# Performance work log

Measured on AMD Instinct MI355X. Metric: run time of the kernel, lower is better.

## Reference

```python
import jax, jax.numpy as jnp
import numpy as np

N_NODES = 100000


def _sage_conv(x, src, dst, W_l, b_l, W_r, n_nodes):
    # mean-aggregate neighbor features: messages flow src -> dst
    msg = x[src]                                              # [E, d]
    agg_sum = jax.ops.segment_sum(msg, dst, num_segments=n_nodes)   # [N, d]
    cnt = jax.ops.segment_sum(jnp.ones((src.shape[0],), x.dtype), dst,
                              num_segments=n_nodes)           # [N]
    agg = agg_sum / jnp.maximum(cnt, 1.0)[:, None]            # mean, 0 for isolated nodes
    return agg @ W_l + b_l + x @ W_r                          # lin_l(agg) + lin_r(x)


def setup_inputs() -> dict:
    key = jax.random.key(0)
    ks = jax.random.split(key, 8)
    in_c, hid_c, out_c = 64, 128, 64
    n_edges = 1000000
    x = jax.random.normal(ks[0], (N_NODES, in_c), dtype=jnp.float32)
    edge_index = jax.random.randint(ks[1], (2, n_edges), 0, N_NODES, dtype=jnp.int32)
    def glorot(k, shape):
        lim = float(np.sqrt(6.0 / (shape[0] + shape[1])))
        return jax.random.uniform(k, shape, jnp.float32, -lim, lim)
    return {
        "x": x,
        "edge_index": edge_index,
        "W_l1": glorot(ks[2], (in_c, hid_c)),
        "b_l1": jnp.zeros((hid_c,), jnp.float32),
        "W_r1": glorot(ks[3], (in_c, hid_c)),
        "W_l2": glorot(ks[4], (hid_c, out_c)),
        "b_l2": jnp.zeros((out_c,), jnp.float32),
        "W_r2": glorot(ks[5], (hid_c, out_c)),
    }


def reference(x, edge_index, W_l1, b_l1, W_r1, W_l2, b_l2, W_r2):
    src, dst = edge_index[0], edge_index[1]
    # eval mode: dropout(p=0.5) is identity
    h = _sage_conv(x, src, dst, W_l1, b_l1, W_r1, N_NODES)
    h = jax.nn.relu(h)
    out = _sage_conv(h, src, dst, W_l2, b_l2, W_r2, N_NODES)
    return out
```

## Files before the change

kernel.cpp:

```cpp
#include <hip/hip_runtime.h>


#define NPB 128
#define NBK 782
#define BCAP_E 1600
#define BCAP_S 2048

typedef __attribute__((ext_vector_type(8))) short bf16x8;
typedef __attribute__((ext_vector_type(4))) float f32x4;
typedef __attribute__((ext_vector_type(4))) int int4v;

__device__ __forceinline__ float bf2f(unsigned short u) {
  return __uint_as_float(((unsigned)u) << 16);
}
__device__ __forceinline__ unsigned short f2bf(float f) {
  unsigned x = __float_as_uint(f);
  x += 0x7fffu + ((x >> 16) & 1u);
  return (unsigned short)(x >> 16);
}

__global__ __launch_bounds__(256) void fused_misc(
    const float* __restrict__ x, unsigned short* __restrict__ xb, int total4,
    const float* __restrict__ Wl1, const float* __restrict__ Wr1,
    const float* __restrict__ Wl2, const float* __restrict__ Wr2,
    unsigned short* __restrict__ Wt1, unsigned short* __restrict__ Wcat,
    int* __restrict__ gcnt, unsigned short* __restrict__ agg1b,
    int n, int CB) {
  int b = blockIdx.x;
  if (b < CB) {
    int i = b * 256 + threadIdx.x;
    if (i < total4) {
      float4 v = ((const float4*)x)[i];
      ushort4 o;
      o.x = f2bf(v.x); o.y = f2bf(v.y); o.z = f2bf(v.z); o.w = f2bf(v.w);
      ((ushort4*)xb)[i] = o;
    }
  } else if (b < CB + 128) {
    int o = (b - CB) * 256 + threadIdx.x;
    if (o < 16384) {
      int m = o >> 13, rem = o & 8191;
      int col = rem >> 6, k = rem & 63;
      const float* W = m ? Wr1 : Wl1;
      Wt1[o] = f2bf(W[k * 128 + col]);
    } else {
      int o2 = o - 16384;
      int col = o2 >> 7, k = o2 & 127;
      float v = (col < 64) ? Wl2[k * 64 + col] : Wr2[k * 64 + col - 64];
      Wcat[o2] = f2bf(v);
    }
  } else {
    for (int i = threadIdx.x; i < NBK; i += 256) gcnt[i] = 0;
    if (threadIdx.x < 32) {
      ((unsigned*)(xb + (size_t)n * 64))[threadIdx.x] = 0;
      ((unsigned*)(agg1b + (size_t)n * 64))[threadIdx.x] = 0;
    }
  }
}

__global__ __launch_bounds__(256) void bucketize(
    const int* __restrict__ src, const int* __restrict__ dst,
    int* __restrict__ gcnt, int* __restrict__ ebuf, int e) {
  __shared__ int lcnt[NBK], lbase[NBK];
  for (int i = threadIdx.x; i < NBK; i += 256) lcnt[i] = 0;
  __syncthreads();
  int pk[16], bk[16];
  int nv = 0;
  int base = blockIdx.x * 4096 + threadIdx.x * 4;
#pragma unroll
  for (int c = 0; c < 4; ++c) {
    int i = base + c * 1024;
    if (i + 4 <= e) {
      int4v sv = *(const int4v*)(src + i);
      int4v dv = *(const int4v*)(dst + i);
#pragma unroll
      for (int j = 0; j < 4; ++j) {
        bk[nv] = dv[j] >> 7;
        pk[nv] = ((dv[j] & 127) << 17) | sv[j];
        ++nv;
      }
    } else if (i < e) {
      for (int i2 = i; i2 < e; ++i2) {
        int dj = dst[i2], sj = src[i2];
        bk[nv] = dj >> 7;
        pk[nv] = ((dj & 127) << 17) | sj;
        ++nv;
      }
    }
  }
  for (int k = 0; k < nv; ++k) atomicAdd(&lcnt[bk[k]], 1);
  __syncthreads();
  for (int i = threadIdx.x; i < NBK; i += 256) {
    lbase[i] = atomicAdd(&gcnt[i], lcnt[i]);
    lcnt[i] = 0;
  }
  __syncthreads();
  for (int k = 0; k < nv; ++k) {
    int off = lbase[bk[k]] + atomicAdd(&lcnt[bk[k]], 1);
    if (off < BCAP_E) ebuf[bk[k] * BCAP_E + off] = pk[k];
  }
}

__global__ __launch_bounds__(256) void sort_write(
    const int* __restrict__ gcnt, const int* __restrict__ ebuf,
    int* __restrict__ srcS, int* __restrict__ nstart, int* __restrict__ ncnt,
    int n) {
  __shared__ int cnt[NPB], cur[NPB], st[NPB + 1], sorted[BCAP_S];
  int tid = threadIdx.x, lane = tid & 63, wid = tid >> 6;
  int b = blockIdx.x;
  if (tid < NPB) { cnt[tid] = 0; cur[tid] = 0; }
  __syncthreads();
  int ecnt = min(gcnt[b], BCAP_E);
  const int* eb = ebuf + b * BCAP_E;
  for (int i = tid; i < ecnt; i += 256) atomicAdd(&cnt[eb[i] >> 17], 1);
  __syncthreads();
  if (wid == 0) {
    int i0 = (cnt[lane] + 3) & ~3, i1 = (cnt[64 + lane] + 3) & ~3;
#pragma unroll
    for (int off = 1; off < 64; off <<= 1) {
      int u = __shfl_up(i0, off);
      if (lane >= off) i0 += u;
    }
    int t0 = __shfl(i0, 63);
#pragma unroll
    for (int off = 1; off < 64; off <<= 1) {
      int u = __shfl_up(i1, off);
      if (lane >= off) i1 += u;
    }
    st[lane + 1] = i0;
    st[64 + lane + 1] = t0 + i1;
    if (lane == 0) st[0] = 0;
  }
  __syncthreads();
  for (int i = tid; i < ecnt; i += 256) {
    int pk = eb[i];
    int dl = pk >> 17;
    int pos = st[dl] + atomicAdd(&cur[dl], 1);
    if (pos < BCAP_S) sorted[pos] = pk & 0x1FFFF;
  }
  __syncthreads();
  if (tid < NPB) {
    int c = cnt[tid], p = (c + 3) & ~3;
    int base = st[tid];
    for (int k = c; k < p; ++k)
      if (base + k < BCAP_S) sorted[base + k] = n;
  }
  __syncthreads();
  int total = min(st[NPB], BCAP_S);
  for (int i = tid; i < total; i += 256) srcS[b * BCAP_S + i] = sorted[i];
  if (tid < NPB) {
    int node = b * NPB + tid;
    if (node < n) {
      nstart[node] = b * BCAP_S + st[tid];
      ncnt[node] = cnt[tid];
    }
  }
}

__device__ __forceinline__ void gather2(
    const unsigned short* __restrict__ feat, const int* __restrict__ srcS,
    int s, int dpad, int lane, float* acc) {
  int half32 = lane & 32;
  int hlane = lane & 31;
  int g = hlane >> 3;
  int ch8 = lane & 7;
#pragma unroll
  for (int j = 0; j < 8; ++j) acc[j] = 0.f;
  int nit = dpad >> 2;
  int nitw = max(nit, __shfl_xor(nit, 32));
  int idx = srcS[s + hlane];
  bf16x8 c[8];
#pragma unroll
  for (int u = 0; u < 8; ++u) {
    if (u < nitw) {
      int r = u * 4 + g;
      int sidx = __shfl(idx, half32 + r);
      if (u < nit) c[u] = *(const bf16x8*)(feat + (size_t)sidx * 64 + ch8 * 8);
    }
  }
#pragma unroll
  for (int u = 0; u < 8; ++u) {
    if (u < nitw && u < nit) {
#pragma unroll
      for (int j = 0; j < 8; ++j) acc[j] += bf2f((unsigned short)c[u][j]);
    }
  }
  for (int b0 = 32; b0 < dpad; b0 += 32) {
    int idx2 = srcS[s + b0 + hlane];
#pragma unroll
    for (int u = 0; u < 8; ++u) {
      int r = u * 4 + g;
      if (b0 + r < dpad) {
        int sidx = __shfl(idx2, half32 + r);
        bf16x8 v = *(const bf16x8*)(feat + (size_t)sidx * 64 + ch8 * 8);
#pragma unroll
        for (int j = 0; j < 8; ++j) acc[j] += bf2f((unsigned short)v[j]);
      }
    }
  }
#pragma unroll
  for (int m = 8; m < 32; m <<= 1) {
#pragma unroll
    for (int j = 0; j < 8; ++j) acc[j] += __shfl_xor(acc[j], m);
  }
}

__global__ __launch_bounds__(256) void agg_mean_fast(
    const unsigned short* __restrict__ feat, const int* __restrict__ nstart,
    const int* __restrict__ ncnt, const int* __restrict__ srcS,
    unsigned short* __restrict__ outp, int n) {
  int lane = threadIdx.x & 63, wid = threadIdx.x >> 6;
  int half = lane >> 5;
  int node = (blockIdx.x * 4 + wid) * 2 + half;
  bool live = node < n;
  int cn = live ? node : n - 1;
  int s = nstart[cn];
  int c = ncnt[cn];
  int dpad = (c + 3) & ~3;
  float acc[8];
  gather2(feat, srcS, s, dpad, lane, acc);
  float inv = 1.f / (float)max(c, 1);
  if ((lane & 31) < 8 && live) {
    bf16x8 o;
#pragma unroll
    for (int j = 0; j < 8; ++j) o[j] = (short)f2bf(acc[j] * inv);
    *(bf16x8*)(outp + (size_t)node * 64 + (lane & 7) * 8) = o;
  }
}

__global__ __launch_bounds__(256) void agg_add_fast(
    const unsigned short* __restrict__ feat, const int* __restrict__ nstart,
    const int* __restrict__ ncnt, const int* __restrict__ srcS,
    float* __restrict__ outp, int n) {
  int lane = threadIdx.x & 63, wid = threadIdx.x >> 6;
  int half = lane >> 5;
  int node = (blockIdx.x * 4 + wid) * 2 + half;
  bool live = node < n;
  int cn = live ? node : n - 1;
  int s = nstart[cn];
  int c = ncnt[cn];
  int dpad = (c + 3) & ~3;
  float acc[8];
  gather2(feat, srcS, s, dpad, lane, acc);
  float inv = 1.f / (float)max(c, 1);
  if ((lane & 31) < 8 && live) {
    float4* op = (float4*)(outp + (size_t)node * 64 + (lane & 7) * 8);
    float4 o0 = op[0], o1 = op[1];
    o0.x += acc[0] * inv; o0.y += acc[1] * inv;
    o0.z += acc[2] * inv; o0.w += acc[3] * inv;
    o1.x += acc[4] * inv; o1.y += acc[5] * inv;
    o1.z += acc[6] * inv; o1.w += acc[7] * inv;
    op[0] = o0; op[1] = o1;
  }
}

__global__ __launch_bounds__(256) void gemm1_mfma(
    const unsigned short* __restrict__ agg, const unsigned short* __restrict__ xb,
    const unsigned short* __restrict__ Wt1, const float* __restrict__ b1,
    unsigned short* __restrict__ h, int n) {
  __shared__ unsigned short sW[16384];
  int tid = threadIdx.x;
  int lane = tid & 63, wid = tid >> 6;
  int l15 = lane & 15, g = lane >> 4;
#pragma unroll
  for (int it = 0; it < 8; ++it) {
    int i = it * 256 + tid;
    int byte = i << 4;
    int col = (byte >> 7) & 127;
    int koff = (byte & 127) ^ ((col & 7) << 4);
    int dstb = (byte & ~127) | koff;
    bf16x8 v = *(const bf16x8*)(Wt1 + i * 8);
    *(bf16x8*)((char*)sW + dstb) = v;
  }
  float bj[8];
#pragma unroll
  for (int cb = 0; cb < 8; ++cb) bj[cb] = b1[cb * 16 + l15];
  __syncthreads();

  int rowbase = blockIdx.x * 128 + wid * 32;
  int r0 = rowbase + l15, r1 = r0 + 16;
  size_t cr0 = (size_t)min(r0, n - 1), cr1 = (size_t)min(r1, n - 1);

  f32x4 acc[2][8];
#pragma unroll
  for (int fr = 0; fr < 2; ++fr)
#pragma unroll
    for (int cb = 0; cb < 8; ++cb) acc[fr][cb] = (f32x4){0.f, 0.f, 0.f, 0.f};

#pragma unroll
  for (int m = 0; m < 2; ++m) {
    const char* base = m ? (const char*)xb : (const char*)agg;
#pragma unroll
    for (int s = 0; s < 2; ++s) {
      int ko = s * 64 + g * 16;
      bf16x8 a0 = *(const bf16x8*)(base + cr0 * 128 + ko);
      bf16x8 a1 = *(const bf16x8*)(base + cr1 * 128 + ko);
#pragma unroll
      for (int cb = 0; cb < 8; ++cb) {
        int col = cb * 16 + l15;
        int koff = ko ^ ((col & 7) << 4);
        bf16x8 b = *(const bf16x8*)((const char*)sW + m * 16384 + col * 128 + koff);
        acc[0][cb] = __builtin_amdgcn_mfma_f32_16x16x32_bf16(a0, b, acc[0][cb], 0, 0, 0);
        acc[1][cb] = __builtin_amdgcn_mfma_f32_16x16x32_bf16(a1, b, acc[1][cb], 0, 0, 0);
      }
    }
  }
#pragma unroll
  for (int fr = 0; fr < 2; ++fr) {
    int rb = rowbase + fr * 16 + g * 4;
#pragma unroll
    for (int r = 0; r < 4; ++r) {
      int row = rb + r;
      if (row < n) {
        unsigned short* hp = h + (size_t)row * 128 + l15;
#pragma unroll
        for (int cb = 0; cb < 8; ++cb) {
          float v = fmaxf(acc[fr][cb][r] + bj[cb], 0.f);
          hp[cb * 16] = f2bf(v);
        }
      }
    }
  }
}

__global__ __launch_bounds__(256) void gemm2_mfma(
    const unsigned short* __restrict__ h, const unsigned short* __restrict__ Wcat,
    const float* __restrict__ b2, unsigned short* __restrict__ t,
    float* __restrict__ outp, int n) {
  __shared__ unsigned short sW[16384];
  int tid = threadIdx.x;
  int lane = tid & 63, wid = tid >> 6;
  int l15 = lane & 15, g = lane >> 4;
#pragma unroll
  for (int it = 0; it < 8; ++it) {
    int i = it * 256 + tid;
    int byte = i << 4;
    int col = byte >> 8;
    int koff = (byte & 255) ^ ((col & 15) << 4);
    int dstb = (byte & ~255) | koff;
    bf16x8 v = *(const bf16x8*)(Wcat + i * 8);
    *(bf16x8*)((char*)sW + dstb) = v;
  }
  float bj[4];
#pragma unroll
  for (int cb = 0; cb < 4; ++cb) bj[cb] = b2[cb * 16 + l15];
  __syncthreads();

  int rowbase = blockIdx.x * 128 + wid * 32;
  int r0 = rowbase + l15, r1 = r0 + 16;
  size_t cr0 = (size_t)min(r0, n - 1), cr1 = (size_t)min(r1, n - 1);

  f32x4 acc[2][8];
#pragma unroll
  for (int fr = 0; fr < 2; ++fr)
#pragma unroll
    for (int cb = 0; cb < 8; ++cb) acc[fr][cb] = (f32x4){0.f, 0.f, 0.f, 0.f};

  const char* hb = (const char*)h;
#pragma unroll
  for (int s = 0; s < 4; ++s) {
    int ko = s * 64 + g * 16;
    bf16x8 a0 = *(const bf16x8*)(hb + cr0 * 256 + ko);
    bf16x8 a1 = *(const bf16x8*)(hb + cr1 * 256 + ko);
#pragma unroll
    for (int cb = 0; cb < 8; ++cb) {
      int col = cb * 16 + l15;
      int koff = ko ^ ((col & 15) << 4);
      bf16x8 b = *(const bf16x8*)((const char*)sW + col * 256 + koff);
      acc[0][cb] = __builtin_amdgcn_mfma_f32_16x16x32_bf16(a0, b, acc[0][cb], 0, 0, 0);
      acc[1][cb] = __builtin_amdgcn_mfma_f32_16x16x32_bf16(a1, b, acc[1][cb], 0, 0, 0);
    }
  }
#pragma unroll
  for (int fr = 0; fr < 2; ++fr) {
    int rb = rowbase + fr * 16 + g * 4;
#pragma unroll
    for (int r = 0; r < 4; ++r) {
      int row = rb + r;
      if (row < n) {
#pragma unroll
        for (int cb = 0; cb < 4; ++cb)
          t[(size_t)row * 64 + cb * 16 + l15] = f2bf(acc[fr][cb][r]);
#pragma unroll
        for (int cb = 0; cb < 4; ++cb)
          outp[(size_t)row * 64 + cb * 16 + l15] = acc[fr][cb + 4][r] + bj[cb];
      }
    }
  }
}

extern "C" void kernel_launch(void* const* d_in, const int* in_sizes, int n_in,
                              void* d_out, int out_size, void* d_ws, size_t ws_size,
                              hipStream_t stream) {
  const float* x   = (const float*)d_in[0];
  const int*   ei  = (const int*)d_in[1];
  const float* Wl1 = (const float*)d_in[2];
  const float* b1  = (const float*)d_in[3];
  const float* Wr1 = (const float*)d_in[4];
  const float* Wl2 = (const float*)d_in[5];
  const float* b2  = (const float*)d_in[6];
  const float* Wr2 = (const float*)d_in[7];
  float* out = (float*)d_out;

  const int n = in_sizes[0] / 64;
  const int e = in_sizes[1] / 2;
  const int* src = ei;
  const int* dst = ei + e;

  char* ws = (char*)d_ws;
  size_t off = 0;
  auto take = [&](size_t bytes) { void* p = ws + off; off = (off + bytes + 255) & ~(size_t)255; return p; };
  int*            gcnt   = (int*)take((size_t)NBK * 4);
  int*            ebuf   = (int*)take((size_t)NBK * BCAP_E * 4);
  int*            srcS   = (int*)take((size_t)NBK * BCAP_S * 4 + 256);
  int*            nstart = (int*)take((size_t)n * 4);
  int*            ncnt   = (int*)take((size_t)n * 4);
  unsigned short* xb     = (unsigned short*)take(((size_t)n + 1) * 64 * 2);
  unsigned short* agg1b  = (unsigned short*)take(((size_t)n + 1) * 64 * 2);
  unsigned short* h      = (unsigned short*)take((size_t)n * 128 * 2);
  unsigned short* t      = agg1b;
  unsigned short* Wt1    = (unsigned short*)take(16384 * 2);
  unsigned short* Wcat   = (unsigned short*)take(16384 * 2);

  const int NTILE = (n + 127) / 128;
  const int total4 = n * 64 / 4;
  const int CB = (total4 + 255) / 256;

  fused_misc<<<CB + 128 + 1, 256, 0, stream>>>(x, xb, total4,
                                               Wl1, Wr1, Wl2, Wr2, Wt1, Wcat,
                                               gcnt, agg1b, n, CB);
  bucketize<<<(e + 4095) / 4096, 256, 0, stream>>>(src, dst, gcnt, ebuf, e);
  sort_write<<<NBK, 256, 0, stream>>>(gcnt, ebuf, srcS, nstart, ncnt, n);

  agg_mean_fast<<<(n + 7) / 8, 256, 0, stream>>>(xb, nstart, ncnt, srcS, agg1b, n);
  gemm1_mfma<<<NTILE, 256, 0, stream>>>(agg1b, xb, Wt1, b1, h, n);

  gemm2_mfma<<<NTILE, 256, 0, stream>>>(h, Wcat, b2, t, out, n);
  agg_add_fast<<<(n + 7) / 8, 256, 0, stream>>>(t, nstart, ncnt, srcS, out, n);
}
```

Baseline: 115.9 us.

## Fuse sort, mean-gather and first GEMM; fold bucketize into prep kernel

New measurement: 124.0 us. 1.07x slower.

```diff
diff --git a/kernel.cpp b/kernel.cpp
--- a/kernel.cpp
+++ b/kernel.cpp
@@ -19,13 +19,16 @@
   return (unsigned short)(x >> 16);
 }
 
-__global__ __launch_bounds__(256) void fused_misc(
+__global__ __launch_bounds__(256) void prep_all(
     const float* __restrict__ x, unsigned short* __restrict__ xb, int total4,
     const float* __restrict__ Wl1, const float* __restrict__ Wr1,
     const float* __restrict__ Wl2, const float* __restrict__ Wr2,
     unsigned short* __restrict__ Wt1, unsigned short* __restrict__ Wcat,
-    int* __restrict__ gcnt, unsigned short* __restrict__ agg1b,
+    unsigned short* __restrict__ tzero,
+    const int* __restrict__ src, const int* __restrict__ dst,
+    int* __restrict__ gcnt, int* __restrict__ ebuf, int e,
     int n, int CB) {
+  __shared__ int lcnt[NBK], lbase[NBK];
   int b = blockIdx.x;
   if (b < CB) {
     int i = b * 256 + threadIdx.x;
@@ -35,7 +38,9 @@
       o.x = f2bf(v.x); o.y = f2bf(v.y); o.z = f2bf(v.z); o.w = f2bf(v.w);
       ((ushort4*)xb)[i] = o;
     }
-  } else if (b < CB + 128) {
+    return;
+  }
+  if (b < CB + 128) {
     int o = (b - CB) * 256 + threadIdx.x;
     if (o < 16384) {
       int m = o >> 13, rem = o & 8191;
@@ -48,24 +53,21 @@
       float v = (col < 64) ? Wl2[k * 64 + col] : Wr2[k * 64 + col - 64];
       Wcat[o2] = f2bf(v);
     }
-  } else {
-    for (int i = threadIdx.x; i < NBK; i += 256) gcnt[i] = 0;
+    return;
+  }
+  if (b < CB + 129) {
     if (threadIdx.x < 32) {
       ((unsigned*)(xb + (size_t)n * 64))[threadIdx.x] = 0;
-      ((unsigned*)(agg1b + (size_t)n * 64))[threadIdx.x] = 0;
-    }
-  }
-}
-
-__global__ __launch_bounds__(256) void bucketize(
-    const int* __restrict__ src, const int* __restrict__ dst,
-    int* __restrict__ gcnt, int* __restrict__ ebuf, int e) {
-  __shared__ int lcnt[NBK], lbase[NBK];
+      ((unsigned*)(tzero + (size_t)n * 64))[threadIdx.x] = 0;
+    }
+    return;
+  }
+  int bb = b - (CB + 129);
   for (int i = threadIdx.x; i < NBK; i += 256) lcnt[i] = 0;
   __syncthreads();
   int pk[16], bk[16];
   int nv = 0;
-  int base = blockIdx.x * 4096 + threadIdx.x * 4;
+  int base = bb * 4096 + threadIdx.x * 4;
 #pragma unroll
   for (int c = 0; c < 4; ++c) {
     int i = base + c * 1024;
@@ -100,18 +102,39 @@
   }
 }
 
-__global__ __launch_bounds__(256) void sort_write(
-    const int* __restrict__ gcnt, const int* __restrict__ ebuf,
+__global__ __launch_bounds__(512) void sort_gather_gemm1(
+    const unsigned short* __restrict__ xb, const int* __restrict__ gcnt,
+    const int* __restrict__ ebuf, const unsigned short* __restrict__ Wt1,
+    const float* __restrict__ b1,
     int* __restrict__ srcS, int* __restrict__ nstart, int* __restrict__ ncnt,
-    int n) {
-  __shared__ int cnt[NPB], cur[NPB], st[NPB + 1], sorted[BCAP_S];
+    unsigned short* __restrict__ h, int n) {
+  __shared__ unsigned short sW[16384];
+  __shared__ unsigned short sA[8192];
+  __shared__ int sorted[BCAP_S];
+  __shared__ int cnt[NPB], cur[NPB], st[NPB + 1];
   int tid = threadIdx.x, lane = tid & 63, wid = tid >> 6;
+  int l15 = lane & 15, g = lane >> 4;
   int b = blockIdx.x;
+
+#pragma unroll
+  for (int it = 0; it < 4; ++it) {
+    int i = it * 512 + tid;
+    int byte = i << 4;
+    int col = (byte >> 7) & 127;
+    int koff = (byte & 127) ^ ((col & 7) << 4);
+    int dstb = (byte & ~127) | koff;
+    bf16x8 v = *(const bf16x8*)(Wt1 + i * 8);
+    *(bf16x8*)((char*)sW + dstb) = v;
+  }
+  float bj[8];
+#pragma unroll
+  for (int cb = 0; cb < 8; ++cb) bj[cb] = b1[cb * 16 + l15];
+
   if (tid < NPB) { cnt[tid] = 0; cur[tid] = 0; }
   __syncthreads();
   int ecnt = min(gcnt[b], BCAP_E);
   const int* eb = ebuf + b * BCAP_E;
-  for (int i = tid; i < ecnt; i += 256) atomicAdd(&cnt[eb[i] >> 17], 1);
+  for (int i = tid; i < ecnt; i += 512) atomicAdd(&cnt[eb[i] >> 17], 1);
   __syncthreads();
   if (wid == 0) {
     int i0 = (cnt[lane] + 3) & ~3, i1 = (cnt[64 + lane] + 3) & ~3;
@@ -131,7 +154,7 @@
     if (lane == 0) st[0] = 0;
   }
   __syncthreads();
-  for (int i = tid; i < ecnt; i += 256) {
+  for (int i = tid; i < ecnt; i += 512) {
     int pk = eb[i];
     int dl = pk >> 17;
     int pos = st[dl] + atomicAdd(&cur[dl], 1);
@@ -143,15 +166,184 @@
     int base = st[tid];
     for (int k = c; k < p; ++k)
       if (base + k < BCAP_S) sorted[base + k] = n;
-  }
-  __syncthreads();
-  int total = min(st[NPB], BCAP_S);
-  for (int i = tid; i < total; i += 256) srcS[b * BCAP_S + i] = sorted[i];
-  if (tid < NPB) {
     int node = b * NPB + tid;
     if (node < n) {
-      nstart[node] = b * BCAP_S + st[tid];
-      ncnt[node] = cnt[tid];
+      nstart[node] = b * BCAP_S + base;
+      ncnt[node] = c;
+    }
+  }
+  __syncthreads();
+  int total = min(st[NPB], BCAP_S);
+  for (int i = tid; i < total; i += 512) srcS[b * BCAP_S + i] = sorted[i];
+
+  {
+    int half32 = lane & 32;
+    int hlane = lane & 31;
+    int gg = hlane >> 3;
+    int ch8 = lane & 7;
+#pragma unroll 1
+    for (int pass = 0; pass < 8; ++pass) {
+      int dl = pass * 16 + wid * 2 + (lane >> 5);
+      int s = st[dl], c = cnt[dl];
+      int dpad = (c + 3) & ~3;
+      float acc[8];
+#pragma unroll
+      for (int j = 0; j < 8; ++j) acc[j] = 0.f;
+      int nit = dpad >> 2;
+      int nitw = max(nit, __shfl_xor(nit, 32));
+      int idx = (s + hlane < BCAP_S) ? sorted[s + hlane] : n;
+      bf16x8 cch[8];
+#pragma unroll
+      for (int u = 0; u < 8; ++u) {
+        if (u < nitw) {
+          int r = u * 4 + gg;
+          int sidx = __shfl(idx, half32 + r);
+          if (u < nit) cch[u] = *(const bf16x8*)(xb + (size_t)sidx * 64 + ch8 * 8);
+        }
+      }
+#pragma unroll
+      for (int u = 0; u < 8; ++u) {
+        if (u < nitw && u < nit) {
+#pragma unroll
+          for (int j = 0; j < 8; ++j) acc[j] += bf2f((unsigned short)cch[u][j]);
+        }
+      }
+      for (int b0 = 32; b0 < dpad; b0 += 32) {
+        int idx2 = (s + b0 + hlane < BCAP_S) ? sorted[s + b0 + hlane] : n;
+#pragma unroll
+        for (int u = 0; u < 8; ++u) {
+          int r = u * 4 + gg;
+          if (b0 + r < dpad) {
+            int sidx = __shfl(idx2, half32 + r);
+            bf16x8 v = *(const bf16x8*)(xb + (size_t)sidx * 64 + ch8 * 8);
+#pragma unroll
+            for (int j = 0; j < 8; ++j) acc[j] += bf2f((unsigned short)v[j]);
+          }
+        }
+      }
+#pragma unroll
+      for (int m = 8; m < 32; m <<= 1) {
+#pragma unroll
+        for (int j = 0; j < 8; ++j) acc[j] += __shfl_xor(acc[j], m);
+      }
+      if (hlane < 8) {
+        float inv = 1.f / (float)max(c, 1);
+        bf16x8 o;
+#pragma unroll
+        for (int j = 0; j < 8; ++j) o[j] = (short)f2bf(acc[j] * inv);
+        int byte = dl * 128 + ((ch8 * 16) ^ ((dl & 7) << 4));
+        *(bf16x8*)((char*)sA + byte) = o;
+      }
+    }
+  }
+  __syncthreads();
+
+  int rowl = wid * 16 + l15;
+  int growbase = b * 128 + wid * 16;
+  size_t cr = (size_t)min(growbase + l15, n - 1);
+
+  f32x4 acc[8];
+#pragma unroll
+  for (int cb = 0; cb < 8; ++cb) acc[cb] = (f32x4){0.f, 0.f, 0.f, 0.f};
+
+#pragma unroll
+  for (int m = 0; m < 2; ++m) {
+#pragma unroll
+    for (int s = 0; s < 2; ++s) {
+      int ko = s * 64 + g * 16;
+      bf16x8 a;
+      if (m == 0) {
+        int koff = ko ^ ((rowl & 7) << 4);
+        a = *(const bf16x8*)((const char*)sA + rowl * 128 + koff);
+      } else {
+        a = *(const bf16x8*)((const char*)xb + cr * 128 + ko);
+      }
+#pragma unroll
+      for (int cb = 0; cb < 8; ++cb) {
+        int col = cb * 16 + l15;
+        int koff = ko ^ ((col & 7) << 4);
+        bf16x8 bb = *(const bf16x8*)((const char*)sW + m * 16384 + col * 128 + koff);
+        acc[cb] = __builtin_amdgcn_mfma_f32_16x16x32_bf16(a, bb, acc[cb], 0, 0, 0);
+      }
+    }
+  }
+  int rb = growbase + g * 4;
+#pragma unroll
+  for (int r = 0; r < 4; ++r) {
+    int row = rb + r;
+    if (row < n) {
+      unsigned short* hp = h + (size_t)row * 128 + l15;
+#pragma unroll
+      for (int cb = 0; cb < 8; ++cb) {
+        float v = fmaxf(acc[cb][r] + bj[cb], 0.f);
+        hp[cb * 16] = f2bf(v);
+      }
+    }
+  }
+}
+
+__global__ __launch_bounds__(256) void gemm2_mfma(
+    const unsigned short* __restrict__ h, const unsigned short* __restrict__ Wcat,
+    const float* __restrict__ b2, unsigned short* __restrict__ t,
+    float* __restrict__ outp, int n) {
+  __shared__ unsigned short sW[16384];
+  int tid = threadIdx.x;
+  int lane = tid & 63, wid = tid >> 6;
+  int l15 = lane & 15, g = lane >> 4;
+#pragma unroll
+  for (int it = 0; it < 8; ++it) {
+    int i = it * 256 + tid;
+    int byte = i << 4;
+    int col = byte >> 8;
+    int koff = (byte & 255) ^ ((col & 15) << 4);
+    int dstb = (byte & ~255) | koff;
+    bf16x8 v = *(const bf16x8*)(Wcat + i * 8);
+    *(bf16x8*)((char*)sW + dstb) = v;
+  }
+  float bj[4];
+#pragma unroll
+  for (int cb = 0; cb < 4; ++cb) bj[cb] = b2[cb * 16 + l15];
+  __syncthreads();
+
+  int rowbase = blockIdx.x * 128 + wid * 32;
+  int r0 = rowbase + l15, r1 = r0 + 16;
+  size_t cr0 = (size_t)min(r0, n - 1), cr1 = (size_t)min(r1, n - 1);
+
+  f32x4 acc[2][8];
+#pragma unroll
+  for (int fr = 0; fr < 2; ++fr)
+#pragma unroll
+    for (int cb = 0; cb < 8; ++cb) acc[fr][cb] = (f32x4){0.f, 0.f, 0.f, 0.f};
+
+  const char* hb = (const char*)h;
+#pragma unroll
+  for (int s = 0; s < 4; ++s) {
+    int ko = s * 64 + g * 16;
+    bf16x8 a0 = *(const bf16x8*)(hb + cr0 * 256 + ko);
+    bf16x8 a1 = *(const bf16x8*)(hb + cr1 * 256 + ko);
+#pragma unroll
+    for (int cb = 0; cb < 8; ++cb) {
+      int col = cb * 16 + l15;
+      int koff = ko ^ ((col & 15) << 4);
+      bf16x8 b = *(const bf16x8*)((const char*)sW + col * 256 + koff);
+      acc[0][cb] = __builtin_amdgcn_mfma_f32_16x16x32_bf16(a0, b, acc[0][cb], 0, 0, 0);
+      acc[1][cb] = __builtin_amdgcn_mfma_f32_16x16x32_bf16(a1, b, acc[1][cb], 0, 0, 0);
+    }
+  }
+#pragma unroll
+  for (int fr = 0; fr < 2; ++fr) {
+    int rb = rowbase + fr * 16 + g * 4;
+#pragma unroll
+    for (int r = 0; r < 4; ++r) {
+      int row = rb + r;
+      if (row < n) {
+#pragma unroll
+        for (int cb = 0; cb < 4; ++cb)
+          t[(size_t)row * 64 + cb * 16 + l15] = f2bf(acc[fr][cb][r]);
+#pragma unroll
+        for (int cb = 0; cb < 4; ++cb)
+          outp[(size_t)row * 64 + cb * 16 + l15] = acc[fr][cb + 4][r] + bj[cb];
+      }
     }
   }
 }
@@ -201,29 +393,6 @@
   for (int m = 8; m < 32; m <<= 1) {
 #pragma unroll
     for (int j = 0; j < 8; ++j) acc[j] += __shfl_xor(acc[j], m);
-  }
-}
-
-__global__ __launch_bounds__(256) void agg_mean_fast(
-    const unsigned short* __restrict__ feat, const int* __restrict__ nstart,
-    const int* __restrict__ ncnt, const int* __restrict__ srcS,
-    unsigned short* __restrict__ outp, int n) {
-  int lane = threadIdx.x & 63, wid = threadIdx.x >> 6;
-  int half = lane >> 5;
-  int node = (blockIdx.x * 4 + wid) * 2 + half;
-  bool live = node < n;
-  int cn = live ? node : n - 1;
-  int s = nstart[cn];
-  int c = ncnt[cn];
-  int dpad = (c + 3) & ~3;
-  float acc[8];
-  gather2(feat, srcS, s, dpad, lane, acc);
-  float inv = 1.f / (float)max(c, 1);
-  if ((lane & 31) < 8 && live) {
-    bf16x8 o;
-#pragma unroll
-    for (int j = 0; j < 8; ++j) o[j] = (short)f2bf(acc[j] * inv);
-    *(bf16x8*)(outp + (size_t)node * 64 + (lane & 7) * 8) = o;
   }
 }
 
@@ -253,141 +422,6 @@
   }
 }
 
-__global__ __launch_bounds__(256) void gemm1_mfma(
-    const unsigned short* __restrict__ agg, const unsigned short* __restrict__ xb,
-    const unsigned short* __restrict__ Wt1, const float* __restrict__ b1,
-    unsigned short* __restrict__ h, int n) {
-  __shared__ unsigned short sW[16384];
-  int tid = threadIdx.x;
-  int lane = tid & 63, wid = tid >> 6;
-  int l15 = lane & 15, g = lane >> 4;
-#pragma unroll
-  for (int it = 0; it < 8; ++it) {
-    int i = it * 256 + tid;
-    int byte = i << 4;
-    int col = (byte >> 7) & 127;
-    int koff = (byte & 127) ^ ((col & 7) << 4);
-    int dstb = (byte & ~127) | koff;
-    bf16x8 v = *(const bf16x8*)(Wt1 + i * 8);
-    *(bf16x8*)((char*)sW + dstb) = v;
-  }
-  float bj[8];
-#pragma unroll
-  for (int cb = 0; cb < 8; ++cb) bj[cb] = b1[cb * 16 + l15];
-  __syncthreads();
-
-  int rowbase = blockIdx.x * 128 + wid * 32;
-  int r0 = rowbase + l15, r1 = r0 + 16;
-  size_t cr0 = (size_t)min(r0, n - 1), cr1 = (size_t)min(r1, n - 1);
-
-  f32x4 acc[2][8];
-#pragma unroll
-  for (int fr = 0; fr < 2; ++fr)
-#pragma unroll
-    for (int cb = 0; cb < 8; ++cb) acc[fr][cb] = (f32x4){0.f, 0.f, 0.f, 0.f};
-
-#pragma unroll
-  for (int m = 0; m < 2; ++m) {
-    const char* base = m ? (const char*)xb : (const char*)agg;
-#pragma unroll
-    for (int s = 0; s < 2; ++s) {
-      int ko = s * 64 + g * 16;
-      bf16x8 a0 = *(const bf16x8*)(base + cr0 * 128 + ko);
-      bf16x8 a1 = *(const bf16x8*)(base + cr1 * 128 + ko);
-#pragma unroll
-      for (int cb = 0; cb < 8; ++cb) {
-        int col = cb * 16 + l15;
-        int koff = ko ^ ((col & 7) << 4);
-        bf16x8 b = *(const bf16x8*)((const char*)sW + m * 16384 + col * 128 + koff);
-        acc[0][cb] = __builtin_amdgcn_mfma_f32_16x16x32_bf16(a0, b, acc[0][cb], 0, 0, 0);
-        acc[1][cb] = __builtin_amdgcn_mfma_f32_16x16x32_bf16(a1, b, acc[1][cb], 0, 0, 0);
-      }
-    }
-  }
-#pragma unroll
-  for (int fr = 0; fr < 2; ++fr) {
-    int rb = rowbase + fr * 16 + g * 4;
-#pragma unroll
-    for (int r = 0; r < 4; ++r) {
-      int row = rb + r;
-      if (row < n) {
-        unsigned short* hp = h + (size_t)row * 128 + l15;
-#pragma unroll
-        for (int cb = 0; cb < 8; ++cb) {
-          float v = fmaxf(acc[fr][cb][r] + bj[cb], 0.f);
-          hp[cb * 16] = f2bf(v);
-        }
-      }
-    }
-  }
-}
-
-__global__ __launch_bounds__(256) void gemm2_mfma(
-    const unsigned short* __restrict__ h, const unsigned short* __restrict__ Wcat,
-    const float* __restrict__ b2, unsigned short* __restrict__ t,
-    float* __restrict__ outp, int n) {
-  __shared__ unsigned short sW[16384];
-  int tid = threadIdx.x;
-  int lane = tid & 63, wid = tid >> 6;
-  int l15 = lane & 15, g = lane >> 4;
-#pragma unroll
-  for (int it = 0; it < 8; ++it) {
-    int i = it * 256 + tid;
-    int byte = i << 4;
-    int col = byte >> 8;
-    int koff = (byte & 255) ^ ((col & 15) << 4);
-    int dstb = (byte & ~255) | koff;
-    bf16x8 v = *(const bf16x8*)(Wcat + i * 8);
-    *(bf16x8*)((char*)sW + dstb) = v;
-  }
-  float bj[4];
-#pragma unroll
-  for (int cb = 0; cb < 4; ++cb) bj[cb] = b2[cb * 16 + l15];
-  __syncthreads();
-
-  int rowbase = blockIdx.x * 128 + wid * 32;
-  int r0 = rowbase + l15, r1 = r0 + 16;
-  size_t cr0 = (size_t)min(r0, n - 1), cr1 = (size_t)min(r1, n - 1);
-
-  f32x4 acc[2][8];
-#pragma unroll
-  for (int fr = 0; fr < 2; ++fr)
-#pragma unroll
-    for (int cb = 0; cb < 8; ++cb) acc[fr][cb] = (f32x4){0.f, 0.f, 0.f, 0.f};
-
-  const char* hb = (const char*)h;
-#pragma unroll
-  for (int s = 0; s < 4; ++s) {
-    int ko = s * 64 + g * 16;
-    bf16x8 a0 = *(const bf16x8*)(hb + cr0 * 256 + ko);
-    bf16x8 a1 = *(const bf16x8*)(hb + cr1 * 256 + ko);
-#pragma unroll
-    for (int cb = 0; cb < 8; ++cb) {
-      int col = cb * 16 + l15;
-      int koff = ko ^ ((col & 15) << 4);
-      bf16x8 b = *(const bf16x8*)((const char*)sW + col * 256 + koff);
-      acc[0][cb] = __builtin_amdgcn_mfma_f32_16x16x32_bf16(a0, b, acc[0][cb], 0, 0, 0);
-      acc[1][cb] = __builtin_amdgcn_mfma_f32_16x16x32_bf16(a1, b, acc[1][cb], 0, 0, 0);
-    }
-  }
-#pragma unroll
-  for (int fr = 0; fr < 2; ++fr) {
-    int rb = rowbase + fr * 16 + g * 4;
-#pragma unroll
-    for (int r = 0; r < 4; ++r) {
-      int row = rb + r;
-      if (row < n) {
-#pragma unroll
-        for (int cb = 0; cb < 4; ++cb)
-          t[(size_t)row * 64 + cb * 16 + l15] = f2bf(acc[fr][cb][r]);
-#pragma unroll
-        for (int cb = 0; cb < 4; ++cb)
-          outp[(size_t)row * 64 + cb * 16 + l15] = acc[fr][cb + 4][r] + bj[cb];
-      }
-    }
-  }
-}
-
 extern "C" void kernel_launch(void* const* d_in, const int* in_sizes, int n_in,
                               void* d_out, int out_size, void* d_ws, size_t ws_size,
                               hipStream_t stream) {
@@ -415,25 +449,21 @@
   int*            nstart = (int*)take((size_t)n * 4);
   int*            ncnt   = (int*)take((size_t)n * 4);
   unsigned short* xb     = (unsigned short*)take(((size_t)n + 1) * 64 * 2);
-  unsigned short* agg1b  = (unsigned short*)take(((size_t)n + 1) * 64 * 2);
+  unsigned short* t      = (unsigned short*)take(((size_t)n + 1) * 64 * 2);
   unsigned short* h      = (unsigned short*)take((size_t)n * 128 * 2);
-  unsigned short* t      = agg1b;
   unsigned short* Wt1    = (unsigned short*)take(16384 * 2);
   unsigned short* Wcat   = (unsigned short*)take(16384 * 2);
 
-  const int NTILE = (n + 127) / 128;
   const int total4 = n * 64 / 4;
   const int CB = (total4 + 255) / 256;
-
-  fused_misc<<<CB + 128 + 1, 256, 0, stream>>>(x, xb, total4,
+  const int EB2 = (e + 4095) / 4096;
+
+  (void)hipMemsetAsync(gcnt, 0, (size_t)NBK * 4, stream);
+  prep_all<<<CB + 129 + EB2, 256, 0, stream>>>(x, xb, total4,
                                                Wl1, Wr1, Wl2, Wr2, Wt1, Wcat,
-                                               gcnt, agg1b, n, CB);
-  bucketize<<<(e + 4095) / 4096, 256, 0, stream>>>(src, dst, gcnt, ebuf, e);
-  sort_write<<<NBK, 256, 0, stream>>>(gcnt, ebuf, srcS, nstart, ncnt, n);
-
-  agg_mean_fast<<<(n + 7) / 8, 256, 0, stream>>>(xb, nstart, ncnt, srcS, agg1b, n);
-  gemm1_mfma<<<NTILE, 256, 0, stream>>>(agg1b, xb, Wt1, b1, h, n);
-
-  gemm2_mfma<<<NTILE, 256, 0, stream>>>(h, Wcat, b2, t, out, n);
+                                               t, src, dst, gcnt, ebuf, e, n, CB);
+  sort_gather_gemm1<<<NBK, 512, 0, stream>>>(xb, gcnt, ebuf, Wt1, b1,
+                                             srcS, nstart, ncnt, h, n);
+  gemm2_mfma<<<NBK, 256, 0, stream>>>(h, Wcat, b2, t, out, n);
   agg_add_fast<<<(n + 7) / 8, 256, 0, stream>>>(t, nstart, ncnt, srcS, out, n);
 }
```
